# Kernel optimization log

Measured on AMD Instinct MI355X. Metric: run time of the kernel, lower is better.

## Reference

```python
import jax, jax.numpy as jnp
import numpy as np

N_USERS = 100000
N_ITEMS = 50000
N = N_USERS + N_ITEMS
EMBED_DIM = 64
N_LAYERS = 3
NNZ = 4800000


def setup_inputs() -> dict:
    key = jax.random.key(0)
    k1, k2, k3, k4, k5 = jax.random.split(key, 5)
    user_emb = jax.random.normal(k1, (N_USERS, EMBED_DIM), dtype=jnp.float32)
    item_emb = jax.random.normal(k2, (N_ITEMS, EMBED_DIM), dtype=jnp.float32)
    adj_row = jax.random.randint(k3, (NNZ,), 0, N, dtype=jnp.int32)
    adj_col = jax.random.randint(k4, (NNZ,), 0, N, dtype=jnp.int32)
    # normalized adjacency values (positive, small) like D^-1/2 A D^-1/2
    adj_vals = jax.random.uniform(k5, (NNZ,), dtype=jnp.float32) * 0.05
    return {"user_emb": user_emb, "item_emb": item_emb,
            "adj_row": adj_row, "adj_col": adj_col, "adj_vals": adj_vals}


def _spmm(vals, row, col, x):
    # sparse (N,N) @ dense (N,d) via gather + segment_sum
    return jax.ops.segment_sum(vals[:, None] * x[col], row, num_segments=N)


def reference(user_emb, item_emb, adj_row, adj_col, adj_vals):
    all_emb = jnp.concatenate([user_emb, item_emb], axis=0)  # (N, d)
    acc = all_emb  # running sum of layer outputs (fused mean)
    cur = all_emb
    for _ in range(N_LAYERS):
        cur = _spmm(adj_vals, adj_row, adj_col, cur)
        acc = acc + cur
    final_emb = acc / jnp.float32(N_LAYERS + 1)
    return final_emb[:N_USERS], final_emb[N_USERS:]
```

## Files before the change

kernel.cpp:

```cpp
#include <hip/hip_runtime.h>

#define N_USERS 100000
#define N_ITEMS 50000
#define N_TOTAL 150000
#define DIM 64
#define NNZ_C 4800000
#define NELEM (N_TOTAL * DIM)
#define NELEM4 (NELEM / 4)

#define RPB 74
#define NB 2048
#define NBLK 512
#define CHUNK (NNZ_C / NBLK)
#define CAP 4096
#define TILES 32
#define TB (NBLK / TILES)

typedef unsigned short ush;

__device__ __forceinline__ float bf2f(ush u) {
    return __uint_as_float(((unsigned)u) << 16);
}
__device__ __forceinline__ ush f2bf(float f) {
    unsigned u = __float_as_uint(f);
    return (ush)((u + 0x7fffu + ((u >> 16) & 1u)) >> 16);
}

__global__ __launch_bounds__(256) void init_kernel(
    const float4* __restrict__ user, const float4* __restrict__ item,
    ushort4* __restrict__ A16) {
    int i = blockIdx.x * 256 + threadIdx.x;
    if (i >= NELEM4) return;
    const int u4 = N_USERS * DIM / 4;
    float4 v = (i < u4) ? user[i] : item[i - u4];
    ushort4 b;
    b.x = f2bf(v.x); b.y = f2bf(v.y); b.z = f2bf(v.z); b.w = f2bf(v.w);
    A16[i] = b;
}

__global__ __launch_bounds__(1024) void p1_hist(
    const int* __restrict__ row, int* __restrict__ histmat) {
    __shared__ int h[NB];
    int t = threadIdx.x, b = blockIdx.x;
    for (int j = t; j < NB; j += 1024) h[j] = 0;
    __syncthreads();
    int kbeg = b * CHUNK, kend = kbeg + CHUNK;
    for (int k = kbeg + t; k < kend; k += 1024) {
        unsigned r = (unsigned)row[k];
        atomicAdd(&h[r / RPB], 1);
    }
    __syncthreads();
    for (int j = t; j < NB; j += 1024) histmat[b * NB + j] = h[j];
}

__global__ __launch_bounds__(256) void p2a1_tilesum(
    const int* __restrict__ histmat, int* __restrict__ tilesum) {
    int j = blockIdx.x * 256 + threadIdx.x;
    int tile = blockIdx.y;
    int b0 = tile * TB;
    int s = 0;
    #pragma unroll
    for (int i = 0; i < TB; i++) s += histmat[(b0 + i) * NB + j];
    tilesum[tile * NB + j] = s;
}

__global__ __launch_bounds__(256) void p2a2_tilescan(
    const int* __restrict__ tilesum, int* __restrict__ tilebase,
    int* __restrict__ T) {
    int j = blockIdx.x * 256 + threadIdx.x;
    int run = 0;
    #pragma unroll
    for (int t = 0; t < TILES; t++) {
        tilebase[t * NB + j] = run;
        run += tilesum[t * NB + j];
    }
    T[j] = run;
}

__global__ __launch_bounds__(256) void p2a3_expand(
    const int* __restrict__ histmat, const int* __restrict__ tilebase,
    int* __restrict__ basemat) {
    int j = blockIdx.x * 256 + threadIdx.x;
    int tile = blockIdx.y;
    int b0 = tile * TB;
    int run = tilebase[tile * NB + j];
    #pragma unroll
    for (int i = 0; i < TB; i++) {
        basemat[(b0 + i) * NB + j] = run;
        run += histmat[(b0 + i) * NB + j];
    }
}

__global__ __launch_bounds__(1024) void p2b_scan(
    const int* __restrict__ T, int* __restrict__ bucketbase,
    int* __restrict__ rowptr) {
    __shared__ int s[1024];
    int t = threadIdx.x;
    int v0 = T[2 * t], v1 = T[2 * t + 1];
    int pair = v0 + v1;
    s[t] = pair;
    __syncthreads();
    for (int off = 1; off < 1024; off <<= 1) {
        int w = (t >= off) ? s[t - off] : 0;
        __syncthreads();
        s[t] += w;
        __syncthreads();
    }
    int excl = s[t] - pair;
    bucketbase[2 * t] = excl;
    bucketbase[2 * t + 1] = excl + v0;
    if (t == 1023) { bucketbase[NB] = s[t]; rowptr[N_TOTAL] = NNZ_C; }
}

__global__ __launch_bounds__(1024) void p3_scatter(
    const int* __restrict__ row, const int* __restrict__ col,
    const float* __restrict__ vals, const int* __restrict__ histmat,
    const int* __restrict__ basemat, const int* __restrict__ bucketbase,
    uint2* __restrict__ entries) {
    __shared__ int s[1024];
    __shared__ int wp[NB];
    __shared__ int gbase[NB];
    __shared__ uint2 sorted[CHUNK];
    __shared__ int dest[CHUNK];
    int t = threadIdx.x, b = blockIdx.x;

    int c0 = histmat[b * NB + 2 * t];
    int c1 = histmat[b * NB + 2 * t + 1];
    int pair = c0 + c1;
    s[t] = pair;
    __syncthreads();
    for (int off = 1; off < 1024; off <<= 1) {
        int w = (t >= off) ? s[t - off] : 0;
        __syncthreads();
        s[t] += w;
        __syncthreads();
    }
    int excl = s[t] - pair;
    wp[2 * t] = excl;
    wp[2 * t + 1] = excl + c0;
    gbase[2 * t]     = bucketbase[2 * t]     + basemat[b * NB + 2 * t]     - excl;
    gbase[2 * t + 1] = bucketbase[2 * t + 1] + basemat[b * NB + 2 * t + 1] - (excl + c0);
    __syncthreads();

    int kbeg = b * CHUNK, kend = kbeg + CHUNK;
    for (int k = kbeg + t; k < kend; k += 1024) {
        unsigned r = (unsigned)row[k];
        unsigned j = r / RPB;
        unsigned rl = r - j * RPB;
        int pos = atomicAdd(&wp[j], 1);
        sorted[pos] = make_uint2((rl << 18) | (unsigned)col[k],
                                 __float_as_uint(vals[k]));
        dest[pos] = gbase[j] + pos;
    }
    __syncthreads();
    for (int i = t; i < CHUNK; i += 1024)
        entries[dest[i]] = sorted[i];
}

__global__ __launch_bounds__(512) void p4_sort(
    const int* __restrict__ bucketbase, uint2* __restrict__ entries,
    int* __restrict__ rowptr) {
    __shared__ uint2 stage[CAP];
    __shared__ int cnt[128], scanb[128], wp[128];
    int t = threadIdx.x, b = blockIdx.x;
    int base = bucketbase[b];
    int n = bucketbase[b + 1] - base;
    if (n > CAP) n = CAP;
    if (t < 128) cnt[t] = 0;
    __syncthreads();
    for (int i = t; i < n; i += 512) {
        uint2 e = entries[base + i];
        stage[i] = e;
        atomicAdd(&cnt[e.x >> 18], 1);
    }
    __syncthreads();
    if (t < 128) scanb[t] = cnt[t];
    __syncthreads();
    for (int off = 1; off < 128; off <<= 1) {
        int w = 0;
        if (t < 128 && t >= off) w = scanb[t - off];
        __syncthreads();
        if (t < 128) scanb[t] += w;
        __syncthreads();
    }
    if (t < RPB) {
        int excl = scanb[t] - cnt[t];
        wp[t] = excl;
        int rg = b * RPB + t;
        if (rg < N_TOTAL) rowptr[rg] = base + excl;
    }
    __syncthreads();
    for (int i = t; i < n; i += 512) {
        uint2 e = stage[i];
        unsigned rl = e.x >> 18;
        int pos = atomicAdd(&wp[rl], 1);
        ((int2*)entries)[base + pos] =
            make_int2((int)(e.x & 0x3FFFFu), (int)e.y);
    }
}

__global__ __launch_bounds__(256) void spmm_csr_kernel(
    const int* __restrict__ rowptr, const int2* __restrict__ csr,
    const ushort4* __restrict__ x4, ushort4* __restrict__ y4) {
    int gid = blockIdx.x * 256 + threadIdx.x;
    int lane = threadIdx.x & 63;
    int group = lane >> 4;
    int chunk = lane & 15;
    int r = (gid >> 6) * 4 + group;
    if (r >= N_TOTAL) return;
    int start = rowptr[r], end = rowptr[r + 1];
    float4 acc = make_float4(0.f, 0.f, 0.f, 0.f);
    for (int j0 = start; j0 < end; j0 += 16) {
        int j = j0 + chunk;
        int2 pair = make_int2(0, 0);
        if (j < end) pair = csr[j];
        int cnt = min(16, end - j0);
        #pragma unroll 4
        for (int t = 0; t < cnt; t++) {
            int src = group * 16 + t;
            int cc = __shfl(pair.x, src);
            float vv = __int_as_float(__shfl(pair.y, src));
            ushort4 xv = x4[cc * 16 + chunk];
            acc.x += vv * bf2f(xv.x);
            acc.y += vv * bf2f(xv.y);
            acc.z += vv * bf2f(xv.z);
            acc.w += vv * bf2f(xv.w);
        }
    }
    int o = r * 16 + chunk;
    ushort4 yb;
    yb.x = f2bf(acc.x); yb.y = f2bf(acc.y);
    yb.z = f2bf(acc.z); yb.w = f2bf(acc.w);
    y4[o] = yb;
}

__global__ __launch_bounds__(256) void spmm_merge_kernel(
    const int* __restrict__ rowptr, const int2* __restrict__ csr,
    const ushort4* __restrict__ x4 , const ushort4* __restrict__ e0,
    const ushort4* __restrict__ e1, float4* __restrict__ out) {
    int gid = blockIdx.x * 256 + threadIdx.x;
    int lane = threadIdx.x & 63;
    int group = lane >> 4;
    int chunk = lane & 15;
    int r = (gid >> 6) * 4 + group;
    if (r >= N_TOTAL) return;
    int start = rowptr[r], end = rowptr[r + 1];
    float4 acc = make_float4(0.f, 0.f, 0.f, 0.f);
    for (int j0 = start; j0 < end; j0 += 16) {
        int j = j0 + chunk;
        int2 pair = make_int2(0, 0);
        if (j < end) pair = csr[j];
        int cnt = min(16, end - j0);
        #pragma unroll 4
        for (int t = 0; t < cnt; t++) {
            int src = group * 16 + t;
            int cc = __shfl(pair.x, src);
            float vv = __int_as_float(__shfl(pair.y, src));
            ushort4 xv = x4[cc * 16 + chunk];
            acc.x += vv * bf2f(xv.x);
            acc.y += vv * bf2f(xv.y);
            acc.z += vv * bf2f(xv.z);
            acc.w += vv * bf2f(xv.w);
        }
    }
    int o = r * 16 + chunk;
    ushort4 a = e0[o], b = e1[o], c = x4[o];
    float4 oo;
    oo.x = (bf2f(a.x) + bf2f(b.x) + bf2f(c.x) + acc.x) * 0.25f;
    oo.y = (bf2f(a.y) + bf2f(b.y) + bf2f(c.y) + acc.y) * 0.25f;
    oo.z = (bf2f(a.z) + bf2f(b.z) + bf2f(c.z) + acc.z) * 0.25f;
    oo.w = (bf2f(a.w) + bf2f(b.w) + bf2f(c.w) + acc.w) * 0.25f;
    out[o] = oo;
}

extern "C" void kernel_launch(void* const* d_in, const int* in_sizes, int n_in,
                              void* d_out, int out_size, void* d_ws, size_t ws_size,
                              hipStream_t stream) {
    const float* user_emb = (const float*)d_in[0];
    const float* item_emb = (const float*)d_in[1];
    const int*   adj_row  = (const int*)d_in[2];
    const int*   adj_col  = (const int*)d_in[3];
    const float* adj_vals = (const float*)d_in[4];
    float* out = (float*)d_out;

    ush*   A          = (ush*)d_ws;
    ush*   B          = A + NELEM;
    ush*   C          = B + NELEM;
    uint2* entries    = (uint2*)(C + NELEM);
    int*   histmat    = (int*)(entries + NNZ_C);
    int*   basemat    = histmat + NBLK * NB;
    int*   tilesum    = basemat + NBLK * NB;
    int*   tilebase   = tilesum + TILES * NB;
    int*   T          = tilebase + TILES * NB;
    int*   bucketbase = T + NB;
    int*   rowptr     = bucketbase + NB + 1;

    const int eltBlocks  = (NELEM4 + 255) / 256;
    const int spmmBlocks = N_TOTAL / 16;

    init_kernel<<<eltBlocks, 256, 0, stream>>>(
        (const float4*)user_emb, (const float4*)item_emb, (ushort4*)A);
    p1_hist<<<NBLK, 1024, 0, stream>>>(adj_row, histmat);
    p2a1_tilesum<<<dim3(NB / 256, TILES), 256, 0, stream>>>(histmat, tilesum);
    p2a2_tilescan<<<NB / 256, 256, 0, stream>>>(tilesum, tilebase, T);
    p2a3_expand<<<dim3(NB / 256, TILES), 256, 0, stream>>>(histmat, tilebase,
                                                           basemat);
    p2b_scan<<<1, 1024, 0, stream>>>(T, bucketbase, rowptr);
    p3_scatter<<<NBLK, 1024, 0, stream>>>(adj_row, adj_col, adj_vals,
                                          histmat, basemat, bucketbase, entries);
    p4_sort<<<NB, 512, 0, stream>>>(bucketbase, entries, rowptr);

    spmm_csr_kernel<<<spmmBlocks, 256, 0, stream>>>(rowptr, (const int2*)entries,
        (const ushort4*)A, (ushort4*)B);
    spmm_csr_kernel<<<spmmBlocks, 256, 0, stream>>>(rowptr, (const int2*)entries,
        (const ushort4*)B, (ushort4*)C);
    spmm_merge_kernel<<<spmmBlocks, 256, 0, stream>>>(rowptr, (const int2*)entries,
        (const ushort4*)C, (const ushort4*)A, (const ushort4*)B, (float4*)out);
}
```

Baseline: 516.2 us.

## Use more scatter blocks, 16-bit histogram matrices, and fuse the tile/bucket scans

Raises the number of partitioning blocks from 512 to 800, so each scatter block handles a smaller chunk and more blocks are resident. Histogram, base and tile matrices are stored as 16-bit values to cut their memory traffic. The tile scan and the bucket scan are merged into one single-block kernel, which removes a launch and the intermediate T array. The scatter kernel stores a 16-bit bucket index per entry instead of a precomputed 32-bit destination, which shrinks shared memory. The 16-bit counters depend on per-tile and per-bucket counts staying below 65536.

```diff
diff --git a/kernel.cpp b/kernel.cpp
--- a/kernel.cpp
+++ b/kernel.cpp
@@ -10,11 +10,11 @@
 
 #define RPB 74
 #define NB 2048
-#define NBLK 512
+#define NBLK 800
 #define CHUNK (NNZ_C / NBLK)
-#define CAP 4096
 #define TILES 32
 #define TB (NBLK / TILES)
+#define CAP 4096
 
 typedef unsigned short ush;
 
@@ -39,89 +39,82 @@
 }
 
 __global__ __launch_bounds__(1024) void p1_hist(
-    const int* __restrict__ row, int* __restrict__ histmat) {
+    const int* __restrict__ row, ush* __restrict__ histmat) {
     __shared__ int h[NB];
     int t = threadIdx.x, b = blockIdx.x;
     for (int j = t; j < NB; j += 1024) h[j] = 0;
     __syncthreads();
-    int kbeg = b * CHUNK, kend = kbeg + CHUNK;
-    for (int k = kbeg + t; k < kend; k += 1024) {
+    int kbeg = b * CHUNK;
+    for (int k = kbeg + t; k < kbeg + CHUNK; k += 1024) {
         unsigned r = (unsigned)row[k];
         atomicAdd(&h[r / RPB], 1);
     }
     __syncthreads();
-    for (int j = t; j < NB; j += 1024) histmat[b * NB + j] = h[j];
+    for (int j = t; j < NB; j += 1024) histmat[b * NB + j] = (ush)h[j];
 }
 
 __global__ __launch_bounds__(256) void p2a1_tilesum(
-    const int* __restrict__ histmat, int* __restrict__ tilesum) {
+    const ush* __restrict__ histmat, ush* __restrict__ tilesum) {
     int j = blockIdx.x * 256 + threadIdx.x;
-    int tile = blockIdx.y;
-    int b0 = tile * TB;
+    int b0 = blockIdx.y * TB;
     int s = 0;
     #pragma unroll
     for (int i = 0; i < TB; i++) s += histmat[(b0 + i) * NB + j];
-    tilesum[tile * NB + j] = s;
-}
-
-__global__ __launch_bounds__(256) void p2a2_tilescan(
-    const int* __restrict__ tilesum, int* __restrict__ tilebase,
-    int* __restrict__ T) {
+    tilesum[blockIdx.y * NB + j] = (ush)s;
+}
+
+__global__ __launch_bounds__(1024) void p2ab_scan(
+    const ush* __restrict__ tilesum, ush* __restrict__ tilebase,
+    int* __restrict__ bucketbase, int* __restrict__ rowptr) {
+    __shared__ int s[1024];
+    int t = threadIdx.x;
+    int j0 = 2 * t, j1 = 2 * t + 1;
+    int r0 = 0, r1 = 0;
+    #pragma unroll
+    for (int tl = 0; tl < TILES; tl++) {
+        tilebase[tl * NB + j0] = (ush)r0;
+        tilebase[tl * NB + j1] = (ush)r1;
+        r0 += tilesum[tl * NB + j0];
+        r1 += tilesum[tl * NB + j1];
+    }
+    int pair = r0 + r1;
+    s[t] = pair;
+    __syncthreads();
+    for (int off = 1; off < 1024; off <<= 1) {
+        int w = (t >= off) ? s[t - off] : 0;
+        __syncthreads();
+        s[t] += w;
+        __syncthreads();
+    }
+    int excl = s[t] - pair;
+    bucketbase[j0] = excl;
+    bucketbase[j1] = excl + r0;
+    if (t == 1023) { bucketbase[NB] = s[t]; rowptr[N_TOTAL] = NNZ_C; }
+}
+
+__global__ __launch_bounds__(256) void p2a3_expand(
+    const ush* __restrict__ histmat, const ush* __restrict__ tilebase,
+    ush* __restrict__ basemat) {
     int j = blockIdx.x * 256 + threadIdx.x;
-    int run = 0;
-    #pragma unroll
-    for (int t = 0; t < TILES; t++) {
-        tilebase[t * NB + j] = run;
-        run += tilesum[t * NB + j];
-    }
-    T[j] = run;
-}
-
-__global__ __launch_bounds__(256) void p2a3_expand(
-    const int* __restrict__ histmat, const int* __restrict__ tilebase,
-    int* __restrict__ basemat) {
-    int j = blockIdx.x * 256 + threadIdx.x;
-    int tile = blockIdx.y;
-    int b0 = tile * TB;
-    int run = tilebase[tile * NB + j];
+    int b0 = blockIdx.y * TB;
+    int run = tilebase[blockIdx.y * NB + j];
     #pragma unroll
     for (int i = 0; i < TB; i++) {
-        basemat[(b0 + i) * NB + j] = run;
+        basemat[(b0 + i) * NB + j] = (ush)run;
         run += histmat[(b0 + i) * NB + j];
     }
-}
-
-__global__ __launch_bounds__(1024) void p2b_scan(
-    const int* __restrict__ T, int* __restrict__ bucketbase,
-    int* __restrict__ rowptr) {
-    __shared__ int s[1024];
-    int t = threadIdx.x;
-    int v0 = T[2 * t], v1 = T[2 * t + 1];
-    int pair = v0 + v1;
-    s[t] = pair;
-    __syncthreads();
-    for (int off = 1; off < 1024; off <<= 1) {
-        int w = (t >= off) ? s[t - off] : 0;
-        __syncthreads();
-        s[t] += w;
-        __syncthreads();
-    }
-    int excl = s[t] - pair;
-    bucketbase[2 * t] = excl;
-    bucketbase[2 * t + 1] = excl + v0;
-    if (t == 1023) { bucketbase[NB] = s[t]; rowptr[N_TOTAL] = NNZ_C; }
 }
 
 __global__ __launch_bounds__(1024) void p3_scatter(
     const int* __restrict__ row, const int* __restrict__ col,
-    const float* __restrict__ vals, const int* __restrict__ histmat,
-    const int* __restrict__ basemat, const int* __restrict__ bucketbase,
+    const float* __restrict__ vals, const ush* __restrict__ histmat,
+    const ush* __restrict__ basemat, const int* __restrict__ bucketbase,
     uint2* __restrict__ entries) {
     __shared__ int s[1024];
     __shared__ int wp[NB];
     __shared__ int gbase[NB];
     __shared__ uint2 sorted[CHUNK];
-    __shared__ int dest[CHUNK];
+    __shared__ ush jarr[CHUNK];
     int t = threadIdx.x, b = blockIdx.x;
 
     int c0 = histmat[b * NB + 2 * t];
@@ -138,23 +131,23 @@
     int excl = s[t] - pair;
     wp[2 * t] = excl;
     wp[2 * t + 1] = excl + c0;
-    gbase[2 * t]     = bucketbase[2 * t]     + basemat[b * NB + 2 * t]     - excl;
-    gbase[2 * t + 1] = bucketbase[2 * t + 1] + basemat[b * NB + 2 * t + 1] - (excl + c0);
-    __syncthreads();
-
-    int kbeg = b * CHUNK, kend = kbeg + CHUNK;
-    for (int k = kbeg + t; k < kend; k += 1024) {
+    gbase[2 * t]     = bucketbase[2 * t]     + (int)basemat[b * NB + 2 * t]     - excl;
+    gbase[2 * t + 1] = bucketbase[2 * t + 1] + (int)basemat[b * NB + 2 * t + 1] - (excl + c0);
+    __syncthreads();
+
+    int kbeg = b * CHUNK;
+    for (int k = kbeg + t; k < kbeg + CHUNK; k += 1024) {
         unsigned r = (unsigned)row[k];
         unsigned j = r / RPB;
         unsigned rl = r - j * RPB;
         int pos = atomicAdd(&wp[j], 1);
         sorted[pos] = make_uint2((rl << 18) | (unsigned)col[k],
                                  __float_as_uint(vals[k]));
-        dest[pos] = gbase[j] + pos;
+        jarr[pos] = (ush)j;
     }
     __syncthreads();
     for (int i = t; i < CHUNK; i += 1024)
-        entries[dest[i]] = sorted[i];
+        entries[gbase[jarr[i]] + i] = sorted[i];
 }
 
 __global__ __launch_bounds__(512) void p4_sort(
@@ -287,12 +280,11 @@
     ush*   B          = A + NELEM;
     ush*   C          = B + NELEM;
     uint2* entries    = (uint2*)(C + NELEM);
-    int*   histmat    = (int*)(entries + NNZ_C);
-    int*   basemat    = histmat + NBLK * NB;
-    int*   tilesum    = basemat + NBLK * NB;
-    int*   tilebase   = tilesum + TILES * NB;
-    int*   T          = tilebase + TILES * NB;
-    int*   bucketbase = T + NB;
+    ush*   histmat    = (ush*)(entries + NNZ_C);
+    ush*   basemat    = histmat + NBLK * NB;
+    ush*   tilesum    = basemat + NBLK * NB;
+    ush*   tilebase   = tilesum + TILES * NB;
+    int*   bucketbase = (int*)(tilebase + TILES * NB);
     int*   rowptr     = bucketbase + NB + 1;
 
     const int eltBlocks  = (NELEM4 + 255) / 256;
@@ -302,10 +294,9 @@
         (const float4*)user_emb, (const float4*)item_emb, (ushort4*)A);
     p1_hist<<<NBLK, 1024, 0, stream>>>(adj_row, histmat);
     p2a1_tilesum<<<dim3(NB / 256, TILES), 256, 0, stream>>>(histmat, tilesum);
-    p2a2_tilescan<<<NB / 256, 256, 0, stream>>>(tilesum, tilebase, T);
+    p2ab_scan<<<1, 1024, 0, stream>>>(tilesum, tilebase, bucketbase, rowptr);
     p2a3_expand<<<dim3(NB / 256, TILES), 256, 0, stream>>>(histmat, tilebase,
                                                            basemat);
-    p2b_scan<<<1, 1024, 0, stream>>>(T, bucketbase, rowptr);
     p3_scatter<<<NBLK, 1024, 0, stream>>>(adj_row, adj_col, adj_vals,
                                           histmat, basemat, bucketbase, entries);
     p4_sort<<<NB, 512, 0, stream>>>(bucketbase, entries, rowptr);
```

New measurement: 523.9 us. Within noise of the previous version (+1.5%).
